# Optimization experiments

Measured on AMD Instinct MI355X. Metric: run time of the kernel, lower is better.

## Reference

```python
import jax, jax.numpy as jnp
import numpy as np

NBINS = 256
STRENGTH = 100.0
C, H, W = 64, 512, 512


def setup_inputs() -> dict:
    key = jax.random.key(0)
    k1, k2, k3, k4 = jax.random.split(key, 4)
    inp = jax.random.uniform(k1, (1, C, H, W), dtype=jnp.float32)
    tgt = jax.random.uniform(k2, (1, C, H, W), dtype=jnp.float32)
    maskI = jax.random.randint(k3, (1, 1, H, W), 0, 2).astype(jnp.int32)
    maskJ = jax.random.randint(k4, (1, 1, H, W), 0, 2).astype(jnp.int32)
    return {"input": inp, "target": tgt, "maskI": maskI, "maskJ": maskJ}


def _hist_remap(I, J, mI, mJ):
    # I, J: [c, HW] float; mI, mJ: [HW] {0,1} float
    c, hw = I.shape
    nI = mI.sum()
    nJ = mJ.sum()
    big = jnp.float32(1e30)
    # per-channel min/max of masked target values (J[mJ].view(c, nJ).min/max)
    minJ = jnp.min(jnp.where(mJ > 0, J, big), axis=1)   # [c]
    maxJ = jnp.max(jnp.where(mJ > 0, J, -big), axis=1)  # [c]
    step = (maxJ - minJ) / NBINS                          # [c]
    # masked per-channel histogram of target (cu.histogram), scaled by nI/nJ
    binJ = jnp.clip(jnp.floor((J - minJ[:, None]) / jnp.maximum(step[:, None], 1e-12)),
                    0, NBINS - 1).astype(jnp.int32)
    seg = binJ + jnp.arange(c, dtype=jnp.int32)[:, None] * NBINS
    hisJ = jax.ops.segment_sum(jnp.broadcast_to(mJ, (c, hw)).reshape(-1),
                               seg.reshape(-1), num_segments=c * NBINS).reshape(c, NBINS)
    hisJ = hisJ * (nI / nJ)
    cumJ = jnp.cumsum(hisJ, axis=1)                       # [c, nbins]
    # mask input; unmasked pixels -> -1 so they sort to the front (msk_sub trick)
    _I = I * mI - (1.0 - mI)                              # [c, HW]
    idxI = jnp.argsort(_I, axis=1)                        # ascending sort order
    # 1-indexed rank among the nI masked pixels (unmasked ranks <= 0, ignored later)
    rank = jnp.arange(hw, dtype=jnp.float32) - (hw - nI) + 1.0  # [HW]

    def per_ch(cum, his, r, mn, st):
        # CDF inverse: smallest bin b with cum[b] >= rank (cu.hist_remap2)
        b = jnp.clip(jnp.searchsorted(cum, r, side='left'), 0, NBINS - 1)
        lo = cum[b] - his[b]
        ratio = jnp.clip((r - lo) / jnp.maximum(his[b], 1e-12), 0.0, 1.0)
        return mn + (b.astype(jnp.float32) + ratio) * st

    vals = jax.vmap(per_ch)(cumJ, hisJ, jnp.broadcast_to(rank, (c, hw)), minJ, step)  # [c, HW]
    # scatter remapped sorted values back to original pixel positions
    R_sorted = jax.vmap(lambda idx, v: jnp.zeros(hw, dtype=v.dtype).at[idx].set(v))(idxI, vals)
    R = jnp.where(mI > 0, R_sorted, I)
    return R


def reference(input, target, maskI, maskJ):
    _, c, h, w = input.shape
    hw = h * w
    I = input[0].reshape(c, hw)
    J = target[0].reshape(c, hw)
    mI = maskI[0, 0].reshape(hw).astype(jnp.float32)
    mJ = maskJ[0, 0].reshape(hw).astype(jnp.float32)
    R = _hist_remap(I, J, mI, mJ)
    # F.mse_loss(I, R) * strength
    loss = jnp.mean((I - R) ** 2) * STRENGTH
    return loss
```

## Files before the change

### kernel.cpp

```cpp
#include <hip/hip_runtime.h>


#define CN    64
#define HWN   262144
#define NB    256
#define NBUK  8192
#define NBLK  16
#define BPIX  (HWN/NBLK)
#define PT    512
#define XB    64
#define QBUK  (NBUK/4)
#define FXS2  268435456.0f
#define FXSI2 (1.0/268435456.0)

__global__ __launch_bounds__(PT, 4) void k_pass1(
    const float* __restrict__ I, const float* __restrict__ J,
    const int* __restrict__ mI, const int* __restrict__ mJ,
    unsigned* __restrict__ pc, unsigned* __restrict__ qtot,
    unsigned* __restrict__ mnp, unsigned* __restrict__ mxp,
    unsigned* __restrict__ cp, double* __restrict__ qp)
{
  const int c = blockIdx.y, q = blockIdx.x, tid = threadIdx.x;
  const int bid = c*NBLK + q;
  const int wid = tid >> 6, lane = tid & 63;
  __shared__ unsigned buk[NBUK];
  __shared__ unsigned sred[PT];
  __shared__ double   dred[PT/64];
  __shared__ unsigned umn[PT/64], umx[PT/64], uci[PT/64], ucj[PT/64];
  for(int i = tid; i < NBUK; i += PT) buk[i] = 0u;
  __syncthreads();

  const float4* Ic  = (const float4*)(I + (size_t)c*HWN + (size_t)q*BPIX);
  const float4* Jc  = (const float4*)(J + (size_t)c*HWN + (size_t)q*BPIX);
  const int4*   MiQ = (const int4*)(mI + (size_t)q*BPIX);
  const int4*   MjQ = (const int4*)(mJ + (size_t)q*BPIX);

  float qacc = 0.0f;
  unsigned ci = 0, cj = 0;
  unsigned mn = 0x7F800000u, mx = 0u;

  float4 bi[2][2]; int4 bmi[2][2];
  float4 bj[2][2]; int4 bmj[2][2];
  #pragma unroll
  for(int g = 0; g < 2; g++){
    int idx = g*PT + tid;
    bi [0][g] = Ic[idx];  bmi[0][g] = MiQ[idx];
    bj [0][g] = Jc[idx];  bmj[0][g] = MjQ[idx];
  }
  #pragma unroll
  for(int b = 0; b < 4; b++){
    const int cur = b & 1, nxt = cur ^ 1;
    if(b < 3){
      #pragma unroll
      for(int g = 0; g < 2; g++){
        int idx = (2*(b+1) + g)*PT + tid;
        bi [nxt][g] = Ic[idx];  bmi[nxt][g] = MiQ[idx];
        bj [nxt][g] = Jc[idx];  bmj[nxt][g] = MjQ[idx];
      }
    }
    #pragma unroll
    for(int g = 0; g < 2; g++){
      float4 vi4 = bi[cur][g]; int4 mi4 = bmi[cur][g];
      float4 vj4 = bj[cur][g]; int4 mj4 = bmj[cur][g];
      float vv[4] = {vi4.x,vi4.y,vi4.z,vi4.w};
      int   mm[4] = {mi4.x,mi4.y,mi4.z,mi4.w};
      #pragma unroll
      for(int e = 0; e < 4; e++){
        if(mm[e] > 0){
          float v = vv[e];
          int k = (int)(v * (float)NBUK);
          if(k > NBUK-1) k = NBUK-1;
          float dv = v - ((float)k + 0.5f) * (1.0f/(float)NBUK);
          int fx = (int)rintf(dv * FXS2);
          atomicAdd(&buk[k], ((unsigned)fx << 12) + 1u);
          qacc += dv*dv;
          ci++;
        }
      }
      if(mj4.x>0){unsigned u=__float_as_uint(vj4.x); mn=min(mn,u); mx=max(mx,u); cj++;}
      if(mj4.y>0){unsigned u=__float_as_uint(vj4.y); mn=min(mn,u); mx=max(mx,u); cj++;}
      if(mj4.z>0){unsigned u=__float_as_uint(vj4.z); mn=min(mn,u); mx=max(mx,u); cj++;}
      if(mj4.w>0){unsigned u=__float_as_uint(vj4.w); mn=min(mn,u); mx=max(mx,u); cj++;}
    }
  }
  __syncthreads();
  { unsigned* pcb = pc + (size_t)bid * NBUK;
    for(int i = tid; i < NBUK; i += PT) pcb[i] = buk[i]; }

  { unsigned csum = 0;
    #pragma unroll
    for(int j = 0; j < 16; j++) csum += buk[tid*16 + j] & 0xFFFu;
    sred[tid] = csum; __syncthreads();
    for(int s = 64; s > 0; s >>= 1){
      if((tid & 127) < s) sred[tid] += sred[tid + s];
      __syncthreads();
    }
    if((tid & 127) == 0) qtot[bid*4 + (tid >> 7)] = sred[tid];
  }

  double qd = (double)qacc;
  for(int o = 32; o > 0; o >>= 1){
    qd += __shfl_down(qd, o, 64);
    mn  = min(mn, (unsigned)__shfl_down(mn, o, 64));
    mx  = max(mx, (unsigned)__shfl_down(mx, o, 64));
    ci += __shfl_down(ci, o, 64);
    cj += __shfl_down(cj, o, 64);
  }
  if(lane == 0){ dred[wid]=qd; umn[wid]=mn; umx[wid]=mx; uci[wid]=ci; ucj[wid]=cj; }
  __syncthreads();
  if(tid == 0){
    double t = 0.0; unsigned amn=0x7F800000u, amx=0u, aci=0, acj=0;
    for(int w = 0; w < PT/64; w++){
      t += dred[w];
      amn = min(amn, umn[w]); amx = max(amx, umx[w]);
      aci += uci[w]; acj += ucj[w];
    }
    qp[bid] = t;
    mnp[bid] = amn; mxp[bid] = amx;
    if(c == 0){ cp[2*q] = aci; cp[2*q+1] = acj; }
  }
}

__global__ __launch_bounds__(256) void k_histJ(
    const float* __restrict__ J, const int* __restrict__ mJ,
    const unsigned* __restrict__ mnp, const unsigned* __restrict__ mxp,
    unsigned* __restrict__ hisPart, double* __restrict__ lossacc,
    unsigned* __restrict__ donecnt)
{
  const int c = blockIdx.y, xb = blockIdx.x, tid = threadIdx.x;
  if(c == 0 && xb == 0 && tid == 0){ *lossacc = 0.0; *donecnt = 0u; }
  unsigned mnu = 0x7F800000u, mxu = 0u;
  #pragma unroll
  for(int qi = 0; qi < NBLK; qi++){
    mnu = min(mnu, mnp[c*NBLK + qi]);
    mxu = max(mxu, mxp[c*NBLK + qi]);
  }
  float mnv = __uint_as_float(mnu);
  float den = fmaxf((__uint_as_float(mxu) - mnv) / (float)NB, 1e-12f);
  __shared__ unsigned h[NB];
  h[tid] = 0u;
  __syncthreads();
  const int SLICE = HWN/XB;
  const float4* Jc = (const float4*)(J + (size_t)c*HWN + (size_t)xb*SLICE);
  const int4*   Mj = (const int4*)(mJ + (size_t)xb*SLICE);
  #pragma unroll
  for(int it = 0; it < SLICE/1024; ++it){
    int idx = it*256 + tid;
    float4 v4 = Jc[idx]; int4 m4 = Mj[idx];
    float vv[4] = {v4.x,v4.y,v4.z,v4.w};
    int   mm[4] = {m4.x,m4.y,m4.z,m4.w};
    #pragma unroll
    for(int e = 0; e < 4; e++){
      if(mm[e] > 0){
        float bf = floorf((vv[e] - mnv) / den);
        bf = fminf(fmaxf(bf, 0.0f), 255.0f);
        atomicAdd(&h[(int)bf], 1u);
      }
    }
  }
  __syncthreads();
  hisPart[((size_t)c*XB + xb)*NB + tid] = h[tid];
}

__global__ __launch_bounds__(1024) void k_closs(
    const unsigned* __restrict__ pc, const unsigned* __restrict__ qtot,
    const unsigned* __restrict__ hisPart,
    const unsigned* __restrict__ mnp, const unsigned* __restrict__ mxp,
    const unsigned* __restrict__ cp, const double* __restrict__ qp,
    double* __restrict__ lossacc, unsigned* __restrict__ donecnt,
    float* __restrict__ out)
{
  const int c = blockIdx.x >> 2, qt = blockIdx.x & 3, tid = threadIdx.x;
  const int wid = tid >> 6, lane = tid & 63;
  __shared__ float cs[NB], hs[NB];
  __shared__ unsigned hsum[NB];
  __shared__ unsigned qsh[NBLK*4];
  __shared__ unsigned wsum[16];
  __shared__ double red[16];
  __shared__ float sh_mn, sh_st;
  __shared__ unsigned sh_base;

  if(tid < NB){
    unsigned hr = 0u;
    for(int xb = 0; xb < XB; xb++) hr += hisPart[((size_t)c*XB + xb)*NB + tid];
    hsum[tid] = hr;
  } else if(tid < NB + NBLK*4){
    int k = tid - NB;
    qsh[k] = qtot[(c*NBLK + (k >> 2))*4 + (k & 3)];
  }
  __syncthreads();
  if(tid == 0){
    unsigned ciw = 0, cjw = 0;
    for(int qi = 0; qi < NBLK; qi++){ ciw += cp[2*qi]; cjw += cp[2*qi+1]; }
    float ratio = (float)ciw / (float)cjw;
    float cum = 0.0f;
    for(int b = 0; b < NB; b++){
      float hh = (float)hsum[b] * ratio;
      hs[b] = hh;
      cum += hh;
      cs[b] = cum;
    }
    unsigned mnu = 0x7F800000u, mxu = 0u;
    for(int qi = 0; qi < NBLK; qi++){ mnu = min(mnu, mnp[c*NBLK+qi]); mxu = max(mxu, mxp[c*NBLK+qi]); }
    sh_mn = __uint_as_float(mnu);
    sh_st = (__uint_as_float(mxu) - sh_mn) / (float)NB;
    unsigned base = 0;
    for(int s = 0; s < NBLK; s++)
      for(int q2 = 0; q2 < qt; q2++) base += qsh[s*4 + q2];
    sh_base = base;
  }
  __syncthreads();

  unsigned  kk[2] = {0,0};
  long long ss[2] = {0,0};
  for(int sl = 0; sl < NBLK; sl++){
    const uint2* pcb = (const uint2*)(pc + (size_t)(c*NBLK + sl)*NBUK + qt*QBUK) + tid;
    uint2 w = *pcb;
    kk[0] += w.x & 0xFFFu;  ss[0] += (int)w.x >> 12;
    kk[1] += w.y & 0xFFFu;  ss[1] += (int)w.y >> 12;
  }
  unsigned run = kk[0] + kk[1];
  unsigned v = run;
  for(int o = 1; o < 64; o <<= 1){
    unsigned t = __shfl_up(v, o, 64);
    if(lane >= o) v += t;
  }
  if(lane == 63) wsum[wid] = v;
  __syncthreads();
  unsigned wbase = 0;
  for(int w = 0; w < wid; w++) wbase += wsum[w];
  unsigned texcl = sh_base + wbase + (v - run);

  float  mnvf = sh_mn, stepf = sh_st;
  double mnvd = (double)mnvf, stepd = (double)stepf;

  float rf0 = (float)(texcl + 1u);
  int lo = 0, hi = NB;
  while(lo < hi){ int mid = (lo + hi) >> 1; if(cs[mid] < rf0) lo = mid + 1; else hi = mid; }
  int bin = (lo > NB-1) ? NB-1 : lo;

  double acc = 0.0;
  unsigned r = texcl;
  #pragma unroll
  for(int j = 0; j < 2; j++){
    unsigned k = kk[j];
    if(k == 0) continue;
    unsigned ra = r + 1u, rb = r + k; r = rb;
    double sval = 0.0;
    while(ra <= rb){
      while(bin < NB-1 && cs[bin] < (float)ra) bin++;
      float csb = cs[bin], hsb = hs[bin];
      unsigned re = (bin == NB-1) ? rb : min(rb, (unsigned)floorf(csb));
      double lovd = (double)csb - (double)hsb;
      double den2 = fmax((double)hsb, 1e-12);
      double ra_d = (double)ra, re_d = (double)re, nn = (double)(re - ra + 1u);
      double rta = (ra_d - lovd)/den2, rtb = (re_d - lovd)/den2;
      if(hsb > 0.0f && rta >= 0.0 && rtb <= 1.0){
        double sumr = 0.5*(ra_d + re_d)*nn;
        sval += nn*(mnvd + (double)bin*stepd) + stepd*(sumr - nn*lovd)/den2;
      } else {
        for(unsigned rr = ra; rr <= re; rr++){
          float rf = (float)rr;
          float lov = csb - hsb;
          float rt = (rf - lov) / fmaxf(hsb, 1e-12f);
          rt = fminf(fmaxf(rt, 0.0f), 1.0f);
          sval += (double)(mnvf + ((float)bin + rt)*stepf);
        }
      }
      ra = re + 1u;
    }
    double kb   = (double)k;
    double cb   = ((double)(qt*QBUK + tid*2 + j) + 0.5) * (1.0/(double)NBUK);
    double vbar = sval/kb - cb;
    double S    = (double)ss[j] * FXSI2;
    acc += kb*vbar*vbar - 2.0*vbar*S;
  }
  if(qt == 0 && tid == 0){
    double qsum = 0.0;
    for(int qi = 0; qi < NBLK; qi++) qsum += qp[c*NBLK + qi];
    acc += qsum;
  }
  for(int o = 32; o > 0; o >>= 1) acc += __shfl_down(acc, o, 64);
  if(lane == 0) red[wid] = acc;
  __syncthreads();
  if(tid == 0){
    double t = 0.0;
    for(int w = 0; w < 16; w++) t += red[w];
    atomicAdd(lossacc, t);
    __threadfence();
    unsigned old = atomicAdd(donecnt, 1u);
    if(old == (unsigned)(CN*4 - 1)){
      double tot = atomicAdd(lossacc, 0.0);
      out[0] = (float)(tot * (100.0 / (double)((size_t)CN * HWN)));
    }
  }
}

extern "C" void kernel_launch(void* const* d_in, const int* in_sizes, int n_in,
                              void* d_out, int out_size, void* d_ws, size_t ws_size,
                              hipStream_t stream){
  const float* I  = (const float*)d_in[0];
  const float* J  = (const float*)d_in[1];
  const int*   mI = (const int*)d_in[2];
  const int*   mJ = (const int*)d_in[3];
  float* out = (float*)d_out;

  char* base = (char*)d_ws;
  size_t pcB = (size_t)CN * NBLK * NBUK * sizeof(unsigned);
  size_t hpB = (size_t)CN * XB * NB * sizeof(unsigned);
  size_t qtB = (size_t)CN * NBLK * 4 * sizeof(unsigned);
  unsigned* pc      = (unsigned*)base;
  unsigned* hisPart = (unsigned*)(base + pcB);
  unsigned* qtot    = (unsigned*)(base + pcB + hpB);
  char* p = base + pcB + hpB + qtB;
  double*   qp      = (double*)p;   p += (size_t)CN*NBLK*sizeof(double);
  double*   lossacc = (double*)p;   p += sizeof(double);
  unsigned* mnp     = (unsigned*)p; p += (size_t)CN*NBLK*sizeof(unsigned);
  unsigned* mxp     = (unsigned*)p; p += (size_t)CN*NBLK*sizeof(unsigned);
  unsigned* cp      = (unsigned*)p; p += 2*NBLK*sizeof(unsigned);
  unsigned* donecnt = (unsigned*)p;

  k_pass1<<<dim3(NBLK, CN), PT, 0, stream>>>(I, J, mI, mJ, pc, qtot, mnp, mxp, cp, qp);
  k_histJ<<<dim3(XB, CN), 256, 0, stream>>>(J, mJ, mnp, mxp, hisPart, lossacc, donecnt);
  k_closs<<<CN*4, 1024, 0, stream>>>(pc, qtot, hisPart, mnp, mxp, cp, qp, lossacc, donecnt, out);
}
```

Before: 189.1 us.

## Pack masks into bitmasks in a pre-kernel to cut per-channel mask reads

Adds a small kernel that compresses the int32 input and target masks into bit-packed arrays. The histogram and pass-1 kernels then load these bits into shared memory instead of re-reading the full int32 masks for every channel. This is meant to cut the redundant mask traffic and load instructions repeated across 64 channels. The cost is an extra kernel launch and some shared-memory staging.

Result: no change. 189.0 us (-0.0%).

```diff
diff --git a/kernel.cpp b/kernel.cpp
--- a/kernel.cpp
+++ b/kernel.cpp
@@ -13,9 +13,26 @@
 #define FXS2  268435456.0f
 #define FXSI2 (1.0/268435456.0)
 
+__global__ __launch_bounds__(256) void k_bits(
+    const int* __restrict__ mI, const int* __restrict__ mJ,
+    unsigned char* __restrict__ bI, unsigned char* __restrict__ bJ)
+{
+  const int t = blockIdx.x*256 + threadIdx.x;
+  const int4* a = (const int4*)mI + 2*t;
+  int4 x0 = a[0], x1 = a[1];
+  unsigned b = (unsigned)((x0.x>0) | ((x0.y>0)<<1) | ((x0.z>0)<<2) | ((x0.w>0)<<3)
+             | ((x1.x>0)<<4) | ((x1.y>0)<<5) | ((x1.z>0)<<6) | ((x1.w>0)<<7));
+  const int4* c = (const int4*)mJ + 2*t;
+  int4 y0 = c[0], y1 = c[1];
+  unsigned d = (unsigned)((y0.x>0) | ((y0.y>0)<<1) | ((y0.z>0)<<2) | ((y0.w>0)<<3)
+             | ((y1.x>0)<<4) | ((y1.y>0)<<5) | ((y1.z>0)<<6) | ((y1.w>0)<<7));
+  bI[t] = (unsigned char)b;
+  bJ[t] = (unsigned char)d;
+}
+
 __global__ __launch_bounds__(PT, 4) void k_pass1(
     const float* __restrict__ I, const float* __restrict__ J,
-    const int* __restrict__ mI, const int* __restrict__ mJ,
+    const unsigned* __restrict__ bI, const unsigned* __restrict__ bJ,
     unsigned* __restrict__ pc, unsigned* __restrict__ qtot,
     unsigned* __restrict__ mnp, unsigned* __restrict__ mxp,
     unsigned* __restrict__ cp, double* __restrict__ qp)
@@ -24,64 +41,50 @@
   const int bid = c*NBLK + q;
   const int wid = tid >> 6, lane = tid & 63;
   __shared__ unsigned buk[NBUK];
+  __shared__ unsigned smbI[BPIX/32], smbJ[BPIX/32];
   __shared__ unsigned sred[PT];
   __shared__ double   dred[PT/64];
   __shared__ unsigned umn[PT/64], umx[PT/64], uci[PT/64], ucj[PT/64];
   for(int i = tid; i < NBUK; i += PT) buk[i] = 0u;
-  __syncthreads();
-
-  const float4* Ic  = (const float4*)(I + (size_t)c*HWN + (size_t)q*BPIX);
-  const float4* Jc  = (const float4*)(J + (size_t)c*HWN + (size_t)q*BPIX);
-  const int4*   MiQ = (const int4*)(mI + (size_t)q*BPIX);
-  const int4*   MjQ = (const int4*)(mJ + (size_t)q*BPIX);
+  smbI[tid] = bI[q*(BPIX/32) + tid];
+  smbJ[tid] = bJ[q*(BPIX/32) + tid];
+  __syncthreads();
+
+  const float4* Ic = (const float4*)(I + (size_t)c*HWN + (size_t)q*BPIX);
+  const float4* Jc = (const float4*)(J + (size_t)c*HWN + (size_t)q*BPIX);
 
   float qacc = 0.0f;
   unsigned ci = 0, cj = 0;
   unsigned mn = 0x7F800000u, mx = 0u;
-
-  float4 bi[2][2]; int4 bmi[2][2];
-  float4 bj[2][2]; int4 bmj[2][2];
+  const int nsh = (tid & 7) * 4;
+
+  float4 pi[2], pj[2];
+  pi[0] = Ic[tid]; pj[0] = Jc[tid];
   #pragma unroll
-  for(int g = 0; g < 2; g++){
-    int idx = g*PT + tid;
-    bi [0][g] = Ic[idx];  bmi[0][g] = MiQ[idx];
-    bj [0][g] = Jc[idx];  bmj[0][g] = MjQ[idx];
-  }
-  #pragma unroll
-  for(int b = 0; b < 4; b++){
-    const int cur = b & 1, nxt = cur ^ 1;
-    if(b < 3){
-      #pragma unroll
-      for(int g = 0; g < 2; g++){
-        int idx = (2*(b+1) + g)*PT + tid;
-        bi [nxt][g] = Ic[idx];  bmi[nxt][g] = MiQ[idx];
-        bj [nxt][g] = Jc[idx];  bmj[nxt][g] = MjQ[idx];
+  for(int g = 0; g < 8; g++){
+    const int cur = g & 1, nxt = cur ^ 1;
+    if(g < 7){ pi[nxt] = Ic[(g+1)*PT + tid]; pj[nxt] = Jc[(g+1)*PT + tid]; }
+    const unsigned bitsI = (smbI[g*64 + (tid>>3)] >> nsh) & 0xFu;
+    const unsigned bitsJ = (smbJ[g*64 + (tid>>3)] >> nsh) & 0xFu;
+    float4 vi4 = pi[cur], vj4 = pj[cur];
+    float vv[4] = {vi4.x, vi4.y, vi4.z, vi4.w};
+    #pragma unroll
+    for(int e = 0; e < 4; e++){
+      if(bitsI & (1u << e)){
+        float v = vv[e];
+        int k = (int)(v * (float)NBUK);
+        if(k > NBUK-1) k = NBUK-1;
+        float dv = v - ((float)k + 0.5f) * (1.0f/(float)NBUK);
+        int fx = (int)rintf(dv * FXS2);
+        atomicAdd(&buk[k], ((unsigned)fx << 12) + 1u);
+        qacc += dv*dv;
+        ci++;
       }
     }
-    #pragma unroll
-    for(int g = 0; g < 2; g++){
-      float4 vi4 = bi[cur][g]; int4 mi4 = bmi[cur][g];
-      float4 vj4 = bj[cur][g]; int4 mj4 = bmj[cur][g];
-      float vv[4] = {vi4.x,vi4.y,vi4.z,vi4.w};
-      int   mm[4] = {mi4.x,mi4.y,mi4.z,mi4.w};
-      #pragma unroll
-      for(int e = 0; e < 4; e++){
-        if(mm[e] > 0){
-          float v = vv[e];
-          int k = (int)(v * (float)NBUK);
-          if(k > NBUK-1) k = NBUK-1;
-          float dv = v - ((float)k + 0.5f) * (1.0f/(float)NBUK);
-          int fx = (int)rintf(dv * FXS2);
-          atomicAdd(&buk[k], ((unsigned)fx << 12) + 1u);
-          qacc += dv*dv;
-          ci++;
-        }
-      }
-      if(mj4.x>0){unsigned u=__float_as_uint(vj4.x); mn=min(mn,u); mx=max(mx,u); cj++;}
-      if(mj4.y>0){unsigned u=__float_as_uint(vj4.y); mn=min(mn,u); mx=max(mx,u); cj++;}
-      if(mj4.z>0){unsigned u=__float_as_uint(vj4.z); mn=min(mn,u); mx=max(mx,u); cj++;}
-      if(mj4.w>0){unsigned u=__float_as_uint(vj4.w); mn=min(mn,u); mx=max(mx,u); cj++;}
-    }
+    if(bitsJ & 1u){unsigned u=__float_as_uint(vj4.x); mn=min(mn,u); mx=max(mx,u); cj++;}
+    if(bitsJ & 2u){unsigned u=__float_as_uint(vj4.y); mn=min(mn,u); mx=max(mx,u); cj++;}
+    if(bitsJ & 4u){unsigned u=__float_as_uint(vj4.z); mn=min(mn,u); mx=max(mx,u); cj++;}
+    if(bitsJ & 8u){unsigned u=__float_as_uint(vj4.w); mn=min(mn,u); mx=max(mx,u); cj++;}
   }
   __syncthreads();
   { unsigned* pcb = pc + (size_t)bid * NBUK;
@@ -122,7 +125,7 @@
 }
 
 __global__ __launch_bounds__(256) void k_histJ(
-    const float* __restrict__ J, const int* __restrict__ mJ,
+    const float* __restrict__ J, const unsigned* __restrict__ bJ,
     const unsigned* __restrict__ mnp, const unsigned* __restrict__ mxp,
     unsigned* __restrict__ hisPart, double* __restrict__ lossacc,
     unsigned* __restrict__ donecnt)
@@ -137,21 +140,23 @@
   }
   float mnv = __uint_as_float(mnu);
   float den = fmaxf((__uint_as_float(mxu) - mnv) / (float)NB, 1e-12f);
+  const int SLICE = HWN/XB;
   __shared__ unsigned h[NB];
+  __shared__ unsigned smb[SLICE/32];
   h[tid] = 0u;
-  __syncthreads();
-  const int SLICE = HWN/XB;
+  if(tid < SLICE/32) smb[tid] = bJ[xb*(SLICE/32) + tid];
+  __syncthreads();
   const float4* Jc = (const float4*)(J + (size_t)c*HWN + (size_t)xb*SLICE);
-  const int4*   Mj = (const int4*)(mJ + (size_t)xb*SLICE);
+  const int nsh = (tid & 7) * 4;
   #pragma unroll
   for(int it = 0; it < SLICE/1024; ++it){
     int idx = it*256 + tid;
-    float4 v4 = Jc[idx]; int4 m4 = Mj[idx];
+    float4 v4 = Jc[idx];
+    const unsigned bits = (smb[it*32 + (tid>>3)] >> nsh) & 0xFu;
     float vv[4] = {v4.x,v4.y,v4.z,v4.w};
-    int   mm[4] = {m4.x,m4.y,m4.z,m4.w};
     #pragma unroll
     for(int e = 0; e < 4; e++){
-      if(mm[e] > 0){
+      if(bits & (1u << e)){
         float bf = floorf((vv[e] - mnv) / den);
         bf = fminf(fmaxf(bf, 0.0f), 255.0f);
         atomicAdd(&h[(int)bf], 1u);
@@ -318,9 +323,17 @@
   unsigned* mnp     = (unsigned*)p; p += (size_t)CN*NBLK*sizeof(unsigned);
   unsigned* mxp     = (unsigned*)p; p += (size_t)CN*NBLK*sizeof(unsigned);
   unsigned* cp      = (unsigned*)p; p += 2*NBLK*sizeof(unsigned);
-  unsigned* donecnt = (unsigned*)p;
-
-  k_pass1<<<dim3(NBLK, CN), PT, 0, stream>>>(I, J, mI, mJ, pc, qtot, mnp, mxp, cp, qp);
-  k_histJ<<<dim3(XB, CN), 256, 0, stream>>>(J, mJ, mnp, mxp, hisPart, lossacc, donecnt);
-  k_closs<<<CN*4, 1024, 0, stream>>>(pc, qtot, hisPart, mnp, mxp, cp, qp, lossacc, donecnt, out);
-}
+  unsigned* donecnt = (unsigned*)p; p += sizeof(unsigned);
+  size_t off = (size_t)(p - base); off = (off + 15) & ~(size_t)15;
+  unsigned char* bIb = (unsigned char*)(base + off);
+  unsigned char* bJb = bIb + HWN/8;
+
+  k_bits<<<HWN/(8*256), 256, 0, stream>>>(mI, mJ, bIb, bJb);
+  k_pass1<<<dim3(NBLK, CN), PT, 0, stream>>>(I, J, (const unsigned*)bIb,
+                                             (const unsigned*)bJb, pc, qtot,
+                                             mnp, mxp, cp, qp);
+  k_histJ<<<dim3(XB, CN), 256, 0, stream>>>(J, (const unsigned*)bJb, mnp, mxp,
+                                            hisPart, lossacc, donecnt);
+  k_closs<<<CN*4, 1024, 0, stream>>>(pc, qtot, hisPart, mnp, mxp, cp, qp,
+                                     lossacc, donecnt, out);
+}
```
